# Performance work log

Measured on AMD Instinct MI355X. Metric: run time of the kernel, lower is better.

The kernel has to match this reference:

```python
import jax, jax.numpy as jnp
import numpy as np

B, S, H, T, N = 32, 512, 1024, 8, 16


def setup_inputs() -> dict:
    key = jax.random.key(0)
    ks = jax.random.split(key, 16)
    sc = 1.0 / np.sqrt(H)
    f32 = jnp.float32
    return {
        "hidden": jax.random.normal(ks[0], (S, B, H), f32),
        "num_encoder_outputs": jax.random.normal(ks[1], (B, N, H), f32),
        "problem_q": jax.random.normal(ks[2], (B, H), f32),
        # GenerateXQs K/V projections
        "Wk": jax.random.normal(ks[3], (H, H), f32) * sc,
        "bk": jax.random.normal(ks[4], (H,), f32) * sc,
        "Wv": jax.random.normal(ks[5], (H, H), f32) * sc,
        "bv": jax.random.normal(ks[6], (H,), f32) * sc,
        # XToQ K/V projections
        "Wk2": jax.random.normal(ks[7], (H, H), f32) * sc,
        "bk2": jax.random.normal(ks[8], (H,), f32) * sc,
        "Wv2": jax.random.normal(ks[9], (H, H), f32) * sc,
        "bv2": jax.random.normal(ks[10], (H,), f32) * sc,
        # XToQ single-layer LSTM (PyTorch gate order i,f,g,o)
        "W_ih": jax.random.normal(ks[11], (4 * H, H), f32) * sc,
        "W_hh": jax.random.normal(ks[12], (4 * H, H), f32) * sc,
        "b_ih": jax.random.normal(ks[13], (4 * H,), f32) * sc,
        "b_hh": jax.random.normal(ks[14], (4 * H,), f32) * sc,
        "num_xs": T,  # all batch items generate T tokens (required for torch.stack)
    }


def _attend(x_bh, keys_bsh, values_bsh):
    # softmax(x @ K^T) @ V, batched over b
    scores = jnp.einsum("bh,bsh->bs", x_bh, keys_bsh)
    attn = jax.nn.softmax(scores, axis=-1)
    return jnp.einsum("bs,bsh->bh", attn, values_bsh)


def reference(hidden, num_encoder_outputs, problem_q,
              Wk, bk, Wv, bv, Wk2, bk2, Wv2, bv2,
              W_ih, W_hh, b_ih, b_hh, num_xs):
    Tn = int(num_xs)
    hidden2 = jnp.swapaxes(hidden, 0, 1)           # [B,S,H]
    keys = hidden2 @ Wk.T + bk                      # [B,S,H]
    values = hidden2 @ Wv.T + bv                    # [B,S,H]

    def gen_step(x, _):
        xn = _attend(x, keys, values)
        return xn, xn

    if Tn > 1:
        _, rest = jax.lax.scan(gen_step, problem_q, None, length=Tn - 1)  # [T-1,B,H]
        final_xs = jnp.concatenate(
            [problem_q[:, None, :], jnp.swapaxes(rest, 0, 1)], axis=1)    # [B,T,H]
    else:
        final_xs = problem_q[:, None, :]

    # XToQ: parallel attention of each generated x over the (projected) hidden
    keys2 = hidden2 @ Wk2.T + bk2
    values2 = hidden2 @ Wv2.T + bv2
    scores = jnp.einsum("bth,bsh->bts", final_xs, keys2)
    attn = jax.nn.softmax(scores, axis=-1)
    qs = jnp.einsum("bts,bsh->bth", attn, values2)  # [B,T,H]

    if Tn > 1:
        # single-layer LSTM over time (PyTorch gate order: i, f, g, o)
        def lstm_step(carry, x_t):
            h, c = carry
            gates = x_t @ W_ih.T + b_ih + h @ W_hh.T + b_hh  # [B,4H]
            i, f, g, o = jnp.split(gates, 4, axis=-1)
            i, f, o = jax.nn.sigmoid(i), jax.nn.sigmoid(f), jax.nn.sigmoid(o)
            g = jnp.tanh(g)
            c = f * c + i * g
            h = o * jnp.tanh(c)
            return (h, c), h

        h0 = jnp.zeros((qs.shape[0], H), qs.dtype)
        c0 = jnp.zeros((qs.shape[0], H), qs.dtype)
        _, outs = jax.lax.scan(lstm_step, (h0, c0), jnp.swapaxes(qs, 0, 1))  # [T,B,H]
        # original appends out1[0] (the t=0 LSTM output) as an extra token
        final_qs = jnp.concatenate([qs, outs[0][:, None, :]], axis=1)        # [B,T+1,H]
    else:
        final_qs = qs

    updated_hidden = jnp.swapaxes(jnp.concatenate([hidden2, final_xs], axis=1), 0, 1)  # [S+T,B,H]
    updated_nums = jnp.concatenate([num_encoder_outputs, final_xs], axis=1)             # [B,N+T,H]
    return (final_qs, updated_hidden, updated_nums)
```

## Files before the change

kernel.cpp:

```cpp
#include <hip/hip_runtime.h>
#include <math.h>

#define Bn 32
#define Sn 512
#define Hn 1024
#define Tn 8
#define Nn 16
#define Gn 4096

__device__ __forceinline__ float wsum(float v){
#pragma unroll
  for (int off = 32; off; off >>= 1) v += __shfl_xor(v, off);
  return v;
}

__device__ __forceinline__ float dot16(float4 a0, float4 a1, float4 a2, float4 a3,
                                       float4 v0, float4 v1, float4 v2, float4 v3){
  float d = a0.x*v0.x + a0.y*v0.y + a0.z*v0.z + a0.w*v0.w;
  d += a1.x*v1.x + a1.y*v1.y + a1.z*v1.z + a1.w*v1.w;
  d += a2.x*v2.x + a2.y*v2.y + a2.z*v2.z + a2.w*v2.w;
  d += a3.x*v3.x + a3.y*v3.y + a3.z*v3.z + a3.w*v3.w;
  return d;
}


__global__ __launch_bounds__(256) void transpose2(
    const float* __restrict__ Wk, const float* __restrict__ Wk2,
    float* __restrict__ WkT, float* __restrict__ Wk2T){
  __shared__ float tile[32][33];
  const float* in  = blockIdx.z ? Wk2  : Wk;
  float*       outp= blockIdx.z ? Wk2T : WkT;
  int tx = threadIdx.x & 31, ty = threadIdx.x >> 5;
  int c0 = blockIdx.x * 32, r0 = blockIdx.y * 32;
#pragma unroll
  for (int k = 0; k < 4; ++k)
    tile[ty + 8*k][tx] = in[(size_t)(r0 + ty + 8*k) * Hn + c0 + tx];
  __syncthreads();
#pragma unroll
  for (int k = 0; k < 4; ++k)
    outp[(size_t)(c0 + ty + 8*k) * Hn + r0 + tx] = tile[tx][ty + 8*k];
}

__global__ __launch_bounds__(256) void prep(
    const float4* __restrict__ nums, const float4* __restrict__ pq,
    float4* __restrict__ un, float4* __restrict__ xs){
  int n = blockIdx.x, b = blockIdx.y;
  if (n < Nn) un[((size_t)b*(Nn+Tn) + n)*256 + threadIdx.x] = nums[((size_t)b*Nn + n)*256 + threadIdx.x];
  else        xs[((size_t)b*Tn)*256 + threadIdx.x] = pq[(size_t)b*256 + threadIdx.x];
}

__global__ __launch_bounds__(256) void finalize_xs(const float4* __restrict__ xs, float4* __restrict__ uh, float4* __restrict__ un){
  int t = blockIdx.x, b = blockIdx.y;
  float4 v = xs[((size_t)b*Tn + t)*256 + threadIdx.x];
  uh[(((size_t)(Sn + t))*Bn + b)*256 + threadIdx.x] = v;
  un[((size_t)b*(Nn+Tn) + Nn + t)*256 + threadIdx.x] = v;
}

template<int FIRST>
__global__ __launch_bounds__(512, 4) void attend9(
    const float* __restrict__ hidden, const float* __restrict__ xk,
    float* __restrict__ ctxp, float* __restrict__ mlp, float* __restrict__ uh)
{
  const int b = blockIdx.y, p = blockIdx.x;
  const int tid = threadIdx.x, lane = tid & 63, w = tid >> 6;
  __shared__ float sM[8], sL[8];
  __shared__ float sacc[8*1024];

  const float4* xp = (const float4*)(xk + (size_t)b*Hn) + lane;
  float4 q0 = xp[0], q1 = xp[64], q2 = xp[128], q3 = xp[192];

  const int s0 = p*32 + w*4;
  size_t ro[4];
#pragma unroll
  for (int i = 0; i < 4; ++i) ro[i] = ((size_t)(s0+i)*Bn + b)*Hn;
  float4 u[4][4];
#pragma unroll
  for (int i = 0; i < 4; ++i){
    const float4* rp = (const float4*)(hidden + ro[i]) + lane;
    u[i][0]=rp[0]; u[i][1]=rp[64]; u[i][2]=rp[128]; u[i][3]=rp[192];
  }
  if (FIRST){
#pragma unroll
    for (int i = 0; i < 4; ++i){
      float4* wp = (float4*)(uh + ro[i]) + lane;
      wp[0]=u[i][0]; wp[64]=u[i][1]; wp[128]=u[i][2]; wp[192]=u[i][3];
    }
  }
  float d[4];
#pragma unroll
  for (int i = 0; i < 4; ++i) d[i] = dot16(q0,q1,q2,q3, u[i][0],u[i][1],u[i][2],u[i][3]);
#pragma unroll
  for (int off = 32; off; off >>= 1){
#pragma unroll
    for (int i = 0; i < 4; ++i) d[i] += __shfl_xor(d[i], off);
  }
  float mw = fmaxf(fmaxf(d[0], d[1]), fmaxf(d[2], d[3]));
  sM[w] = mw;
  __syncthreads();
  float M = sM[0];
#pragma unroll
  for (int i = 1; i < 8; ++i) M = fmaxf(M, sM[i]);
  float wi[4], lw = 0.f;
#pragma unroll
  for (int i = 0; i < 4; ++i){ wi[i] = __expf(d[i] - M); lw += wi[i]; }
  float4 a0, a1, a2, a3;
  a0 = make_float4(wi[0]*u[0][0].x, wi[0]*u[0][0].y, wi[0]*u[0][0].z, wi[0]*u[0][0].w);
  a1 = make_float4(wi[0]*u[0][1].x, wi[0]*u[0][1].y, wi[0]*u[0][1].z, wi[0]*u[0][1].w);
  a2 = make_float4(wi[0]*u[0][2].x, wi[0]*u[0][2].y, wi[0]*u[0][2].z, wi[0]*u[0][2].w);
  a3 = make_float4(wi[0]*u[0][3].x, wi[0]*u[0][3].y, wi[0]*u[0][3].z, wi[0]*u[0][3].w);
#pragma unroll
  for (int i = 1; i < 4; ++i){
    a0.x = fmaf(wi[i], u[i][0].x, a0.x); a0.y = fmaf(wi[i], u[i][0].y, a0.y);
    a0.z = fmaf(wi[i], u[i][0].z, a0.z); a0.w = fmaf(wi[i], u[i][0].w, a0.w);
    a1.x = fmaf(wi[i], u[i][1].x, a1.x); a1.y = fmaf(wi[i], u[i][1].y, a1.y);
    a1.z = fmaf(wi[i], u[i][1].z, a1.z); a1.w = fmaf(wi[i], u[i][1].w, a1.w);
    a2.x = fmaf(wi[i], u[i][2].x, a2.x); a2.y = fmaf(wi[i], u[i][2].y, a2.y);
    a2.z = fmaf(wi[i], u[i][2].z, a2.z); a2.w = fmaf(wi[i], u[i][2].w, a2.w);
    a3.x = fmaf(wi[i], u[i][3].x, a3.x); a3.y = fmaf(wi[i], u[i][3].y, a3.y);
    a3.z = fmaf(wi[i], u[i][3].z, a3.z); a3.w = fmaf(wi[i], u[i][3].w, a3.w);
  }

  {
    int sl0 = (lane*4 + 0) ^ (lane & 7);
    int sl1 = (lane*4 + 1) ^ (lane & 7);
    int sl2 = (lane*4 + 2) ^ (lane & 7);
    int sl3 = (lane*4 + 3) ^ (lane & 7);
    *(float4*)(sacc + w*1024 + sl0*4) = a0;
    *(float4*)(sacc + w*1024 + sl1*4) = a1;
    *(float4*)(sacc + w*1024 + sl2*4) = a2;
    *(float4*)(sacc + w*1024 + sl3*4) = a3;
  }
  if (lane == 0) sL[w] = lw;
  __syncthreads();
#pragma unroll
  for (int h0 = 0; h0 < 1024; h0 += 512){
    int c = h0 + tid;
    int k = c >> 8, l = (c >> 2) & 63, j = c & 3;
    int fo = ((((l << 2) + k) ^ (l & 7)) << 2) + j;
    float s = 0.f;
#pragma unroll
    for (int i = 0; i < 8; ++i) s += sacc[i*1024 + fo];
    ctxp[((size_t)b*16 + p)*1024 + c] = s;
  }
  if (tid == 0){
    float L = 0.f;
#pragma unroll
    for (int i = 0; i < 8; ++i) L += sL[i];
    mlp[((size_t)b*16 + p)*2]     = M;
    mlp[((size_t)b*16 + p)*2 + 1] = L;
  }
}

__global__ __launch_bounds__(256) void mv1(
    const float* __restrict__ X, int xstride,
    const float* __restrict__ M, float* __restrict__ part,
    int nj, int ktiles)
{
  __shared__ float wt[64*128];
  __shared__ float xl[64*32];
  const int t  = threadIdx.x;
  const int j0 = blockIdx.x * 128;
  const int kb = blockIdx.y;
  const int r0 = blockIdx.z * 32;
  const int R  = gridDim.z * 32;
  const int tj = t & 31, tr = t >> 5;
  float acc[4][4] = {{0.f,0.f,0.f,0.f},{0.f,0.f,0.f,0.f},{0.f,0.f,0.f,0.f},{0.f,0.f,0.f,0.f}};

  for (int kt = 0; kt < ktiles; ++kt){
    const int k0 = (kb*ktiles + kt)*64;
    __syncthreads();
    {
      int j = t >> 1;
      int kqb = (t & 1) * 8;
      const float* Mrow = M + (size_t)(j0 + j)*1024 + k0;
#pragma unroll
      for (int c = 0; c < 8; ++c){
        float4 v = *(const float4*)(Mrow + (kqb + c)*4);
        int kk = (kqb + c)*4;
        wt[(kk+0)*128 + j] = v.x;
        wt[(kk+1)*128 + j] = v.y;
        wt[(kk+2)*128 + j] = v.z;
        wt[(kk+3)*128 + j] = v.w;
      }
      int r = t >> 3;
      int kq0 = t & 7;
#pragma unroll
      for (int c = 0; c < 2; ++c){
        int kk = (kq0 + c*8)*4;
        float4 v = *(const float4*)(X + (size_t)(r0 + r)*xstride + k0 + kk);
        xl[(kk+0)*32 + r] = v.x;
        xl[(kk+1)*32 + r] = v.y;
        xl[(kk+2)*32 + r] = v.z;
        xl[(kk+3)*32 + r] = v.w;
      }
    }
    __syncthreads();
#pragma unroll 4
    for (int k = 0; k < 64; ++k){
      float4 w4 = *(const float4*)(wt + k*128 + tj*4);
      float4 x4 = *(const float4*)(xl + k*32  + tr*4);
      acc[0][0] = fmaf(x4.x, w4.x, acc[0][0]);
      acc[0][1] = fmaf(x4.x, w4.y, acc[0][1]);
      acc[0][2] = fmaf(x4.x, w4.z, acc[0][2]);
      acc[0][3] = fmaf(x4.x, w4.w, acc[0][3]);
      acc[1][0] = fmaf(x4.y, w4.x, acc[1][0]);
      acc[1][1] = fmaf(x4.y, w4.y, acc[1][1]);
      acc[1][2] = fmaf(x4.y, w4.z, acc[1][2]);
      acc[1][3] = fmaf(x4.y, w4.w, acc[1][3]);
      acc[2][0] = fmaf(x4.z, w4.x, acc[2][0]);
      acc[2][1] = fmaf(x4.z, w4.y, acc[2][1]);
      acc[2][2] = fmaf(x4.z, w4.z, acc[2][2]);
      acc[2][3] = fmaf(x4.z, w4.w, acc[2][3]);
      acc[3][0] = fmaf(x4.w, w4.x, acc[3][0]);
      acc[3][1] = fmaf(x4.w, w4.y, acc[3][1]);
      acc[3][2] = fmaf(x4.w, w4.z, acc[3][2]);
      acc[3][3] = fmaf(x4.w, w4.w, acc[3][3]);
    }
  }
  const size_t base = ((size_t)kb*R + r0 + tr*4)*nj + j0 + tj*4;
#pragma unroll
  for (int i = 0; i < 4; ++i)
    *(float4*)(part + base + (size_t)i*nj) = make_float4(acc[i][0], acc[i][1], acc[i][2], acc[i][3]);
}

__global__ __launch_bounds__(256) void mv2(
    const float* __restrict__ part, int R, int njshift, int KB,
    const float* __restrict__ b1, const float* __restrict__ b2,
    float* __restrict__ out, int rpgshift, int opg)
{
  int idx = blockIdx.x*256 + threadIdx.x;
  int nj = 1 << njshift;
  int r = idx >> njshift, j = idx & (nj - 1);
  float s = 0.f;
  if (b1) s += b1[j];
  if (b2) s += b2[j];
  size_t stride = (size_t)R << njshift;
  for (int kb = 0; kb < KB; ++kb) s += part[(size_t)kb*stride + idx];
  int orow = ((r >> rpgshift) * opg) + (r & ((1 << rpgshift) - 1));
  out[((size_t)orow << njshift) + j] = s;
}

__global__ __launch_bounds__(256) void genstep(
    const float* __restrict__ ctxp, const float* __restrict__ mlp,
    const float* __restrict__ Wv, float* __restrict__ part)
{
  __shared__ float wt[64*128];
  __shared__ float xl[64*32];
  const int t  = threadIdx.x;
  const int j0 = blockIdx.x * 128;
  const int kb = blockIdx.y;
  const int k0 = kb*64;
  const int tj = t & 31, tr = t >> 5;

  {
    int j = t >> 1;
    int kqb = (t & 1) * 8;
    const float* Mrow = Wv + (size_t)(j0 + j)*1024 + k0;
#pragma unroll
    for (int c = 0; c < 8; ++c){
      float4 v = *(const float4*)(Mrow + (kqb + c)*4);
      int kk = (kqb + c)*4;
      wt[(kk+0)*128 + j] = v.x;
      wt[(kk+1)*128 + j] = v.y;
      wt[(kk+2)*128 + j] = v.z;
      wt[(kk+3)*128 + j] = v.w;
    }
  }
  {
    int b = t >> 3, kk = (t & 7)*8;
    float mx = -1e30f;
#pragma unroll
    for (int i = 0; i < 16; ++i) mx = fmaxf(mx, mlp[((size_t)b*16 + i)*2]);
    float L = 0.f;
    float a8[8] = {0.f,0.f,0.f,0.f,0.f,0.f,0.f,0.f};
#pragma unroll 4
    for (int i = 0; i < 16; ++i){
      float m = mlp[((size_t)b*16 + i)*2];
      float l = mlp[((size_t)b*16 + i)*2 + 1];
      float we = __expf(m - mx);
      L = fmaf(l, we, L);
      const float* cp = ctxp + ((size_t)b*16 + i)*1024 + k0 + kk;
      float4 u0 = *(const float4*)cp;
      float4 u1 = *(const float4*)(cp + 4);
      a8[0] = fmaf(we, u0.x, a8[0]); a8[1] = fmaf(we, u0.y, a8[1]);
      a8[2] = fmaf(we, u0.z, a8[2]); a8[3] = fmaf(we, u0.w, a8[3]);
      a8[4] = fmaf(we, u1.x, a8[4]); a8[5] = fmaf(we, u1.y, a8[5]);
      a8[6] = fmaf(we, u1.z, a8[6]); a8[7] = fmaf(we, u1.w, a8[7]);
    }
    float inv = 1.f / L;
#pragma unroll
    for (int q = 0; q < 8; ++q) xl[(kk + q)*32 + b] = a8[q]*inv;
  }
  __syncthreads();
  float acc[4][4] = {{0.f,0.f,0.f,0.f},{0.f,0.f,0.f,0.f},{0.f,0.f,0.f,0.f},{0.f,0.f,0.f,0.f}};
#pragma unroll 4
  for (int k = 0; k < 64; ++k){
    float4 w4 = *(const float4*)(wt + k*128 + tj*4);
    float4 x4 = *(const float4*)(xl + k*32  + tr*4);
    acc[0][0] = fmaf(x4.x, w4.x, acc[0][0]);
    acc[0][1] = fmaf(x4.x, w4.y, acc[0][1]);
    acc[0][2] = fmaf(x4.x, w4.z, acc[0][2]);
    acc[0][3] = fmaf(x4.x, w4.w, acc[0][3]);
    acc[1][0] = fmaf(x4.y, w4.x, acc[1][0]);
    acc[1][1] = fmaf(x4.y, w4.y, acc[1][1]);
    acc[1][2] = fmaf(x4.y, w4.z, acc[1][2]);
    acc[1][3] = fmaf(x4.y, w4.w, acc[1][3]);
    acc[2][0] = fmaf(x4.z, w4.x, acc[2][0]);
    acc[2][1] = fmaf(x4.z, w4.y, acc[2][1]);
    acc[2][2] = fmaf(x4.z, w4.z, acc[2][2]);
    acc[2][3] = fmaf(x4.z, w4.w, acc[2][3]);
    acc[3][0] = fmaf(x4.w, w4.x, acc[3][0]);
    acc[3][1] = fmaf(x4.w, w4.y, acc[3][1]);
    acc[3][2] = fmaf(x4.w, w4.z, acc[3][2]);
    acc[3][3] = fmaf(x4.w, w4.w, acc[3][3]);
  }
  const size_t base = ((size_t)kb*32 + tr*4)*1024 + j0 + tj*4;
#pragma unroll
  for (int i = 0; i < 4; ++i)
    *(float4*)(part + base + (size_t)i*1024) = make_float4(acc[i][0], acc[i][1], acc[i][2], acc[i][3]);
}


__global__ __launch_bounds__(512) void scores2_kernel(
    const float* __restrict__ hidden, const float* __restrict__ xk2, float* __restrict__ sc)
{
  int b = blockIdx.y, p = blockIdx.x;
  int lane = threadIdx.x & 63, w = threadIdx.x >> 6;
  int t0 = (w & 3) * 2, rh = w >> 2;
  const float4* qa = (const float4*)(xk2 + ((size_t)b*Tn + t0  )*Hn) + lane;
  const float4* qb = (const float4*)(xk2 + ((size_t)b*Tn + t0+1)*Hn) + lane;
  float4 a0=qa[0], a1=qa[64], a2=qa[128], a3=qa[192];
  float4 c0=qb[0], c1=qb[64], c2=qb[128], c3=qb[192];
#pragma unroll 2
  for (int r = 0; r < 8; ++r){
    int s = p*16 + rh*8 + r;
    const float4* row = (const float4*)(hidden + ((size_t)s*Bn + b)*Hn) + lane;
    float4 v0=row[0], v1=row[64], v2=row[128], v3=row[192];
    float d0 = wsum(dot16(a0,a1,a2,a3, v0,v1,v2,v3));
    float d1 = wsum(dot16(c0,c1,c2,c3, v0,v1,v2,v3));
    if (lane == 0){
      sc[((size_t)b*Tn + t0  )*Sn + s] = d0;
      sc[((size_t)b*Tn + t0+1)*Sn + s] = d1;
    }
  }
}

__global__ __launch_bounds__(512) void softmax512(float* __restrict__ sc){
  int row = blockIdx.x, tid = threadIdx.x, lane = tid & 63, w = tid >> 6;
  float v = sc[(size_t)row*Sn + tid];
  float mx = v;
#pragma unroll
  for (int off = 32; off; off >>= 1) mx = fmaxf(mx, __shfl_xor(mx, off));
  __shared__ float sm[8], ss[8];
  if (lane == 0) sm[w] = mx;
  __syncthreads();
  mx = sm[0];
#pragma unroll
  for (int i = 1; i < 8; ++i) mx = fmaxf(mx, sm[i]);
  float e = __expf(v - mx);
  float s = e;
#pragma unroll
  for (int off = 32; off; off >>= 1) s += __shfl_xor(s, off);
  if (lane == 0) ss[w] = s;
  __syncthreads();
  float tot = 0.f;
#pragma unroll
  for (int i = 0; i < 8; ++i) tot += ss[i];
  sc[(size_t)row*Sn + tid] = e / tot;
}

__global__ __launch_bounds__(512) void ctx2p(
    const float* __restrict__ hidden, const float* __restrict__ attn, float* __restrict__ part)
{
  int hc = blockIdx.x, sc = blockIdx.y, b = blockIdx.z;
  int tid = threadIdx.x, hloc = tid & 127, tg = tid >> 7;
  __shared__ float al[Tn*128];
  for (int idx = tid; idx < Tn*128; idx += 512){
    int t = idx >> 7, si = idx & 127;
    al[idx] = attn[((size_t)b*Tn + t)*Sn + sc*128 + si];
  }
  __syncthreads();
  int h = hc*128 + hloc, t0 = tg*2;
  float acc0 = 0.f, acc1 = 0.f;
#pragma unroll 4
  for (int si = 0; si < 128; ++si){
    int s = sc*128 + si;
    float v = hidden[((size_t)s*Bn + b)*Hn + h];
    acc0 = fmaf(al[t0*128 + si],     v, acc0);
    acc1 = fmaf(al[(t0+1)*128 + si], v, acc1);
  }
  part[(((size_t)sc*Bn + b)*Tn + t0  )*Hn + h] = acc0;
  part[(((size_t)sc*Bn + b)*Tn + t0+1)*Hn + h] = acc1;
}

__global__ __launch_bounds__(256) void ctx2r(const float* __restrict__ part, float* __restrict__ out){
  int idx = blockIdx.x*256 + threadIdx.x;
  out[idx] = part[idx] + part[262144 + idx] + part[524288 + idx] + part[786432 + idx];
}

__global__ __launch_bounds__(256) void lstm_fused(
    const float* __restrict__ part, const float* __restrict__ b_ih,
    const float* __restrict__ b_hh, float* __restrict__ fq)
{
  int idx = blockIdx.x*256 + threadIdx.x;
  int b = idx >> 10, h = idx & 1023;
  const size_t stride = (size_t)32*Gn;
  float gi = b_ih[h] + b_hh[h];
  float gg = b_ih[2048+h] + b_hh[2048+h];
  float go = b_ih[3072+h] + b_hh[3072+h];
  for (int kb = 0; kb < 16; ++kb){
    const float* pp = part + (size_t)kb*stride + (size_t)b*Gn;
    gi += pp[h]; gg += pp[2048+h]; go += pp[3072+h];
  }
  float si = 1.f/(1.f + __expf(-gi));
  float so = 1.f/(1.f + __expf(-go));
  float c  = si * tanhf(gg);
  fq[((size_t)b*(Tn+1) + Tn)*Hn + h] = so * tanhf(c);
}


extern "C" void kernel_launch(void* const* d_in, const int* in_sizes, int n_in,
                              void* d_out, int out_size, void* d_ws, size_t ws_size,
                              hipStream_t stream) {
  const float* hidden = (const float*)d_in[0];
  const float* nums   = (const float*)d_in[1];
  const float* pq     = (const float*)d_in[2];
  const float* Wk     = (const float*)d_in[3];
  const float* Wv     = (const float*)d_in[5];
  const float* bv     = (const float*)d_in[6];
  const float* Wk2    = (const float*)d_in[7];
  const float* Wv2    = (const float*)d_in[9];
  const float* bv2    = (const float*)d_in[10];
  const float* W_ih   = (const float*)d_in[11];
  const float* b_ih   = (const float*)d_in[13];
  const float* b_hh   = (const float*)d_in[14];

  float* out = (float*)d_out;
  float* fq  = out;
  float* uh  = out + (size_t)Bn*(Tn+1)*Hn;
  float* un  = uh + (size_t)(Sn+Tn)*Bn*Hn;

  float* ws    = (float*)d_ws;
  float* xs    = ws;
  float* ctxp  = ws + 262144;
  float* mlp   = ws + 1310720;
  float* xk    = ws + 1312768;
  float* xk2   = ws + 1345536;
  float* sc2   = ws + 1607680;
  float* ctx2v = ws + 1738752;
  float* partX = ws + 2000896;
  float* partK = ws + 2525184;
  float* WkT   = ws + 3049472;
  float* Wk2T  = ws + 4098048;
  float* partS = partX;
  float* c2part= partX;
  float* partL = WkT;

  transpose2<<<dim3(32,32,2), 256, 0, stream>>>(Wk, Wk2, WkT, Wk2T);
  prep<<<dim3(Nn+1, Bn), 256, 0, stream>>>((const float4*)nums, (const float4*)pq, (float4*)un, (float4*)xs);

  mv1<<<dim3(8,16,1), 256, 0, stream>>>(pq, Hn, WkT, partK, Hn, 1);
  mv2<<<128, 256, 0, stream>>>(partK, 32, 10, 16, nullptr, nullptr, xk, 0, 1);

  for (int t = 1; t < Tn; ++t){
    if (t == 1) attend9<1><<<dim3(16,Bn), 512, 0, stream>>>(hidden, xk, ctxp, mlp, uh);
    else        attend9<0><<<dim3(16,Bn), 512, 0, stream>>>(hidden, xk, ctxp, mlp, uh);
    genstep<<<dim3(8,16), 256, 0, stream>>>(ctxp, mlp, Wv, partX);
    mv2<<<128, 256, 0, stream>>>(partX, 32, 10, 16, bv, nullptr, xs + (size_t)t*Hn, 0, Tn);
    if (t < Tn-1){
      mv1<<<dim3(8,16,1), 256, 0, stream>>>(xs + (size_t)t*Hn, Tn*Hn, WkT, partK, Hn, 1);
      mv2<<<128, 256, 0, stream>>>(partK, 32, 10, 16, nullptr, nullptr, xk, 0, 1);
    }
  }

  mv1<<<dim3(8,4,8), 256, 0, stream>>>(xs, Hn, Wk2T, partS, Hn, 4);
  mv2<<<1024, 256, 0, stream>>>(partS, 256, 10, 4, nullptr, nullptr, xk2, 0, 1);
  scores2_kernel<<<dim3(32, Bn), 512, 0, stream>>>(hidden, xk2, sc2);
  softmax512<<<Bn*Tn, 512, 0, stream>>>(sc2);
  ctx2p<<<dim3(8, 4, Bn), 512, 0, stream>>>(hidden, sc2, c2part);
  ctx2r<<<1024, 256, 0, stream>>>(c2part, ctx2v);
  mv1<<<dim3(8,4,8), 256, 0, stream>>>(ctx2v, Hn, Wv2, partS, Hn, 4);
  mv2<<<1024, 256, 0, stream>>>(partS, 256, 10, 4, bv2, nullptr, fq, 3, Tn+1);

  mv1<<<dim3(32,16,1), 256, 0, stream>>>(fq, (Tn+1)*Hn, W_ih, partL, Gn, 1);
  lstm_fused<<<128, 256, 0, stream>>>(partL, b_ih, b_hh, fq);

  finalize_xs<<<dim3(Tn, Bn), 256, 0, stream>>>((const float4*)xs, (float4*)uh, (float4*)un);
}
```

Baseline: 379.7 us.

## Fold Wv and Wk into combined matrix to shorten serial generation chain

Precomputes the product of the Wv and Wk projections as one combined matrix, plus a bias term dk from bv and Wk. Each serial generation step then maps the attention context straight to the next query key with one matvec and reduce, instead of computing the value projection and then the key projection. The value projections for all steps are deferred and done in one batched matvec over the saved contexts after the loop. The aim is fewer serial kernel launches and matvecs on the critical path, at the cost of an up-front 1024x1024x1024 matrix product, an extra transpose and more workspace, with slightly different rounding.

New measurement: 379.7 us. No clear change (-0.0%).

```diff
diff --git a/kernel.cpp b/kernel.cpp
--- a/kernel.cpp
+++ b/kernel.cpp
@@ -24,12 +24,12 @@
 }
 
 
-__global__ __launch_bounds__(256) void transpose2(
-    const float* __restrict__ Wk, const float* __restrict__ Wk2,
-    float* __restrict__ WkT, float* __restrict__ Wk2T){
+__global__ __launch_bounds__(256) void transpose3(
+    const float* __restrict__ Wk, const float* __restrict__ Wk2, const float* __restrict__ Wv,
+    float* __restrict__ WkT, float* __restrict__ Wk2T, float* __restrict__ WvT){
   __shared__ float tile[32][33];
-  const float* in  = blockIdx.z ? Wk2  : Wk;
-  float*       outp= blockIdx.z ? Wk2T : WkT;
+  const float* in  = (blockIdx.z == 0) ? Wk  : (blockIdx.z == 1) ? Wk2  : Wv;
+  float*       outp= (blockIdx.z == 0) ? WkT : (blockIdx.z == 1) ? Wk2T : WvT;
   int tx = threadIdx.x & 31, ty = threadIdx.x >> 5;
   int c0 = blockIdx.x * 32, r0 = blockIdx.y * 32;
 #pragma unroll
@@ -54,6 +54,19 @@
   float4 v = xs[((size_t)b*Tn + t)*256 + threadIdx.x];
   uh[(((size_t)(Sn + t))*Bn + b)*256 + threadIdx.x] = v;
   un[((size_t)b*(Nn+Tn) + Nn + t)*256 + threadIdx.x] = v;
+}
+
+__global__ __launch_bounds__(256) void dkv(
+    const float* __restrict__ bv, const float* __restrict__ WkT, float* __restrict__ dk)
+{
+  int lane = threadIdx.x & 63, w = threadIdx.x >> 6;
+  int j = blockIdx.x*4 + w;
+  const float4* rp = (const float4*)(WkT + (size_t)j*Hn) + lane;
+  const float4* bp = (const float4*)bv + lane;
+  float4 v0=rp[0], v1=rp[64], v2=rp[128], v3=rp[192];
+  float4 b0=bp[0], b1=bp[64], b2=bp[128], b3=bp[192];
+  float d = wsum(dot16(b0,b1,b2,b3, v0,v1,v2,v3));
+  if (lane == 0) dk[j] = d;
 }
 
 template<int FIRST>
@@ -119,7 +132,6 @@
     a3.x = fmaf(wi[i], u[i][3].x, a3.x); a3.y = fmaf(wi[i], u[i][3].y, a3.y);
     a3.z = fmaf(wi[i], u[i][3].z, a3.z); a3.w = fmaf(wi[i], u[i][3].w, a3.w);
   }
-
   {
     int sl0 = (lane*4 + 0) ^ (lane & 7);
     int sl1 = (lane*4 + 1) ^ (lane & 7);
@@ -240,9 +252,10 @@
   out[((size_t)orow << njshift) + j] = s;
 }
 
-__global__ __launch_bounds__(256) void genstep(
+template<int FULL>
+__global__ __launch_bounds__(256) void genw(
     const float* __restrict__ ctxp, const float* __restrict__ mlp,
-    const float* __restrict__ Wv, float* __restrict__ part)
+    const float* __restrict__ D, float* __restrict__ part, float* __restrict__ ctxout)
 {
   __shared__ float wt[64*128];
   __shared__ float xl[64*32];
@@ -252,10 +265,10 @@
   const int k0 = kb*64;
   const int tj = t & 31, tr = t >> 5;
 
-  {
+  if (FULL){
     int j = t >> 1;
     int kqb = (t & 1) * 8;
-    const float* Mrow = Wv + (size_t)(j0 + j)*1024 + k0;
+    const float* Mrow = D + (size_t)(j0 + j)*1024 + k0;
 #pragma unroll
     for (int c = 0; c < 8; ++c){
       float4 v = *(const float4*)(Mrow + (kqb + c)*4);
@@ -289,8 +302,13 @@
     }
     float inv = 1.f / L;
 #pragma unroll
-    for (int q = 0; q < 8; ++q) xl[(kk + q)*32 + b] = a8[q]*inv;
-  }
+    for (int q = 0; q < 8; ++q){
+      float c = a8[q]*inv;
+      if (FULL) xl[(kk + q)*32 + b] = c;
+      if (!FULL || blockIdx.x == 0) ctxout[(size_t)b*1024 + k0 + kk + q] = c;
+    }
+  }
+  if (!FULL) return;
   __syncthreads();
   float acc[4][4] = {{0.f,0.f,0.f,0.f},{0.f,0.f,0.f,0.f},{0.f,0.f,0.f,0.f},{0.f,0.f,0.f,0.f}};
 #pragma unroll 4
@@ -320,6 +338,19 @@
     *(float4*)(part + base + (size_t)i*1024) = make_float4(acc[i][0], acc[i][1], acc[i][2], acc[i][3]);
 }
 
+__global__ __launch_bounds__(256) void mv2xs(
+    const float* __restrict__ part, const float* __restrict__ bv, float* __restrict__ xs)
+{
+  int idx = blockIdx.x*256 + threadIdx.x;
+  int r = idx >> 10, j = idx & 1023;
+  int t = r >> 5, b = r & 31;
+  const size_t stride = (size_t)224*1024;
+  float s = bv[j];
+#pragma unroll
+  for (int kb = 0; kb < 4; ++kb) s += part[(size_t)kb*stride + idx];
+  xs[(((size_t)b*Tn) + t + 1)*1024 + j] = s;
+}
+
 
 __global__ __launch_bounds__(512) void scores2_kernel(
     const float* __restrict__ hidden, const float* __restrict__ xk2, float* __restrict__ sc)
@@ -452,12 +483,18 @@
   float* partK = ws + 2525184;
   float* WkT   = ws + 3049472;
   float* Wk2T  = ws + 4098048;
+  float* WvT   = ws + 5146624;
+  float* Dcomb = ws + 6195200;
+  float* ctxall= ws + 7243776;
+  float* dk    = ws + 7473152;
   float* partS = partX;
   float* c2part= partX;
   float* partL = WkT;
 
-  transpose2<<<dim3(32,32,2), 256, 0, stream>>>(Wk, Wk2, WkT, Wk2T);
+  transpose3<<<dim3(32,32,3), 256, 0, stream>>>(Wk, Wk2, Wv, WkT, Wk2T, WvT);
   prep<<<dim3(Nn+1, Bn), 256, 0, stream>>>((const float4*)nums, (const float4*)pq, (float4*)un, (float4*)xs);
+  mv1<<<dim3(8,1,32), 256, 0, stream>>>(WkT, Hn, WvT, Dcomb, Hn, 16);
+  dkv<<<256, 256, 0, stream>>>(bv, WkT, dk);
 
   mv1<<<dim3(8,16,1), 256, 0, stream>>>(pq, Hn, WkT, partK, Hn, 1);
   mv2<<<128, 256, 0, stream>>>(partK, 32, 10, 16, nullptr, nullptr, xk, 0, 1);
@@ -465,13 +502,17 @@
   for (int t = 1; t < Tn; ++t){
     if (t == 1) attend9<1><<<dim3(16,Bn), 512, 0, stream>>>(hidden, xk, ctxp, mlp, uh);
     else        attend9<0><<<dim3(16,Bn), 512, 0, stream>>>(hidden, xk, ctxp, mlp, uh);
-    genstep<<<dim3(8,16), 256, 0, stream>>>(ctxp, mlp, Wv, partX);
-    mv2<<<128, 256, 0, stream>>>(partX, 32, 10, 16, bv, nullptr, xs + (size_t)t*Hn, 0, Tn);
+    float* ctxt = ctxall + (size_t)(t-1)*Bn*Hn;
     if (t < Tn-1){
-      mv1<<<dim3(8,16,1), 256, 0, stream>>>(xs + (size_t)t*Hn, Tn*Hn, WkT, partK, Hn, 1);
-      mv2<<<128, 256, 0, stream>>>(partK, 32, 10, 16, nullptr, nullptr, xk, 0, 1);
-    }
-  }
+      genw<1><<<dim3(8,16), 256, 0, stream>>>(ctxp, mlp, Dcomb, partX, ctxt);
+      mv2<<<128, 256, 0, stream>>>(partX, 32, 10, 16, dk, nullptr, xk, 0, 1);
+    } else {
+      genw<0><<<dim3(1,16), 256, 0, stream>>>(ctxp, mlp, Dcomb, partX, ctxt);
+    }
+  }
+
+  mv1<<<dim3(8,4,7), 256, 0, stream>>>(ctxall, Hn, Wv, partS, Hn, 4);
+  mv2xs<<<896, 256, 0, stream>>>(partS, bv, xs);
 
   mv1<<<dim3(8,4,8), 256, 0, stream>>>(xs, Hn, Wk2T, partS, Hn, 4);
   mv2<<<1024, 256, 0, stream>>>(partS, 256, 10, 4, nullptr, nullptr, xk2, 0, 1);
```
